# Performance work log

Hardware: AMD Instinct MI355X
Metric: run time of the kernel (lower is better)

## Reference

```python
import jax, jax.numpy as jnp
import numpy as np

EPS = 1e-05


def setup_inputs() -> dict:
    key = jax.random.key(0)
    k1, k2, k3 = jax.random.split(key, 3)
    B, M, W, H = 256, 8192, 32, 4
    memory = jax.random.normal(k1, (B, M, W), dtype=jnp.float32)
    keys = jax.random.normal(k2, (B, H, W), dtype=jnp.float32)
    strengths = jax.random.normal(k3, (B, H), dtype=jnp.float32)
    return {"memory": memory, "keys": keys, "strengths": strengths}


def reference(memory, keys, strengths):
    # memory: [B, M, W], keys: [B, H, W], strengths: [B, H]
    dot = jnp.einsum('bhw,bmw->bhm', keys, memory)          # [B, H, M]
    mem_norms = jnp.sqrt(jnp.sum(memory * memory, axis=-1) + EPS)  # [B, M]
    key_norms = jnp.sqrt(jnp.sum(keys * keys, axis=-1) + EPS)      # [B, H]
    norm = key_norms[:, :, None] * mem_norms[:, None, :]    # [B, H, M]
    activations = dot / (norm + EPS)
    sharp = activations * jax.nn.softplus(strengths)[:, :, None]
    # BatchSoftmax: legacy F.softmax on 2D [H, M] slices -> softmax over M
    return jax.nn.softmax(sharp, axis=-1)
```

## Files before the change

kernel.cpp:

```cpp
#include <hip/hip_runtime.h>
#include <math.h>

#define EPS 1e-5f

constexpr int Mc = 8192;
constexpr int Wc = 32;
constexpr int Hc = 4;
constexpr int NT = 1024;
constexpr int LD = Mc + 8;

__global__ __launch_bounds__(NT, 4) void weightfn_kernel(
    const float* __restrict__ memory,
    const float* __restrict__ keys,
    const float* __restrict__ strengths,
    float* __restrict__ out)
{
    __shared__ __align__(16) float s_sharp[Hc * LD];
    __shared__ __align__(16) float s_key[Hc * Wc];
    __shared__ float s_kn[Hc];
    __shared__ float s_beta[Hc];
    __shared__ float s_redm[NT / 64][Hc];
    __shared__ float s_redl[NT / 64][Hc];
    __shared__ float s_max[Hc];
    __shared__ float s_inv[Hc];

    const int b = blockIdx.x;
    const int t = threadIdx.x;

    if (t < Hc * Wc) s_key[t] = keys[(size_t)b * Hc * Wc + t];
    __syncthreads();
    if (t < Hc) {
        float s = 0.f;
        #pragma unroll
        for (int w = 0; w < Wc; ++w) { float k = s_key[t * Wc + w]; s += k * k; }
        s_kn[t] = sqrtf(s + EPS);
        float x = strengths[(size_t)b * Hc + t];
        s_beta[t] = fmaxf(x, 0.f) + log1pf(expf(-fabsf(x)));
    }
    __syncthreads();

    const int w4 = t & 7;
    const int mg = t >> 3;
    const float4* mp = reinterpret_cast<const float4*>(memory) + (size_t)b * (Mc * Wc / 4);
    const float4* kp = reinterpret_cast<const float4*>(s_key);
    const float4 k0 = kp[0 * 8 + w4];
    const float4 k1 = kp[1 * 8 + w4];
    const float4 k2 = kp[2 * 8 + w4];
    const float4 k3 = kp[3 * 8 + w4];
    const float myKn   = s_kn[w4 & 3];
    const float myBeta = s_beta[w4 & 3];

    #pragma unroll 4
    for (int k = 0; k < Mc / (NT / 8); ++k) {
        const int m = mg + k * (NT / 8);
        float4 v = mp[t + k * NT];
        float sq = v.x * v.x + v.y * v.y + v.z * v.z + v.w * v.w;
        float d0 = v.x * k0.x + v.y * k0.y + v.z * k0.z + v.w * k0.w;
        float d1 = v.x * k1.x + v.y * k1.y + v.z * k1.z + v.w * k1.w;
        float d2 = v.x * k2.x + v.y * k2.y + v.z * k2.z + v.w * k2.w;
        float d3 = v.x * k3.x + v.y * k3.y + v.z * k3.z + v.w * k3.w;
        #pragma unroll
        for (int off = 1; off <= 4; off <<= 1) {
            sq += __shfl_xor(sq, off);
            d0 += __shfl_xor(d0, off);
            d1 += __shfl_xor(d1, off);
            d2 += __shfl_xor(d2, off);
            d3 += __shfl_xor(d3, off);
        }
        if (w4 < Hc) {
            float d = (w4 == 0) ? d0 : (w4 == 1) ? d1 : (w4 == 2) ? d2 : d3;
            float mn = sqrtf(sq + EPS);
            s_sharp[w4 * LD + m] = d * myBeta / (myKn * mn + EPS);
        }
    }
    __syncthreads();

    const int wave = t >> 6;
    const int lane = t & 63;
    float mx[Hc];
    #pragma unroll
    for (int h = 0; h < Hc; ++h) mx[h] = -INFINITY;
    #pragma unroll
    for (int k = 0; k < Mc / NT; ++k) {
        const int m = t + k * NT;
        #pragma unroll
        for (int h = 0; h < Hc; ++h) mx[h] = fmaxf(mx[h], s_sharp[h * LD + m]);
    }
    #pragma unroll
    for (int off = 1; off < 64; off <<= 1) {
        #pragma unroll
        for (int h = 0; h < Hc; ++h) mx[h] = fmaxf(mx[h], __shfl_xor(mx[h], off));
    }
    if (lane == 0) {
        #pragma unroll
        for (int h = 0; h < Hc; ++h) s_redm[wave][h] = mx[h];
    }
    __syncthreads();
    if (t < Hc) {
        float m0 = s_redm[0][t];
        #pragma unroll
        for (int i = 1; i < NT / 64; ++i) m0 = fmaxf(m0, s_redm[i][t]);
        s_max[t] = m0;
    }
    __syncthreads();

    float gm[Hc];
    #pragma unroll
    for (int h = 0; h < Hc; ++h) gm[h] = s_max[h];
    float ls[Hc];
    #pragma unroll
    for (int h = 0; h < Hc; ++h) ls[h] = 0.f;
    #pragma unroll
    for (int k = 0; k < Mc / NT; ++k) {
        const int m = t + k * NT;
        #pragma unroll
        for (int h = 0; h < Hc; ++h) ls[h] += expf(s_sharp[h * LD + m] - gm[h]);
    }
    #pragma unroll
    for (int off = 1; off < 64; off <<= 1) {
        #pragma unroll
        for (int h = 0; h < Hc; ++h) ls[h] += __shfl_xor(ls[h], off);
    }
    if (lane == 0) {
        #pragma unroll
        for (int h = 0; h < Hc; ++h) s_redl[wave][h] = ls[h];
    }
    __syncthreads();
    if (t < Hc) {
        float s = 0.f;
        #pragma unroll
        for (int i = 0; i < NT / 64; ++i) s += s_redl[i][t];
        s_inv[t] = 1.f / s;
    }
    __syncthreads();

    float4* op = reinterpret_cast<float4*>(out) + (size_t)b * (Hc * Mc / 4);
    #pragma unroll
    for (int k = 0; k < (Hc * Mc / 4) / NT; ++k) {
        const int f = t + k * NT;
        const int h = f >> 11;
        const int r = f & 2047;
        float4 v = *reinterpret_cast<const float4*>(&s_sharp[h * LD + r * 4]);
        const float gmh = s_max[h];
        const float gih = s_inv[h];
        float4 o;
        o.x = expf(v.x - gmh) * gih;
        o.y = expf(v.y - gmh) * gih;
        o.z = expf(v.z - gmh) * gih;
        o.w = expf(v.w - gmh) * gih;
        op[f] = o;
    }
}

extern "C" void kernel_launch(void* const* d_in, const int* in_sizes, int n_in,
                              void* d_out, int out_size, void* d_ws, size_t ws_size,
                              hipStream_t stream) {
    const float* memory    = (const float*)d_in[0];
    const float* keys      = (const float*)d_in[1];
    const float* strengths = (const float*)d_in[2];
    float* out = (float*)d_out;

    const int B = in_sizes[0] / (Mc * Wc);
    dim3 grid(B), block(NT);
    hipLaunchKernelGGL(weightfn_kernel, grid, block, 0, stream,
                       memory, keys, strengths, out);
}
```

Baseline: 380.2 us.

## Drop softmax max pass by exploiting bounded cosine-similarity logits

Computes exp of the sharpened cosine similarity directly in the dot-product loop and accumulates the per-head sum there, removing the max-reduction pass, the separate sum pass, and the exp in the output pass. This relies on cosine similarity being bounded in [-1,1] so exp(beta*cos) stays in range when softplus(strength) is moderate. It could overflow for very large strengths. Fast-math intrinsics (__expf, rcp) replace expf and division, trading a little precision for fewer instructions.

```diff
diff --git a/kernel.cpp b/kernel.cpp
--- a/kernel.cpp
+++ b/kernel.cpp
@@ -19,9 +19,7 @@
     __shared__ __align__(16) float s_key[Hc * Wc];
     __shared__ float s_kn[Hc];
     __shared__ float s_beta[Hc];
-    __shared__ float s_redm[NT / 64][Hc];
     __shared__ float s_redl[NT / 64][Hc];
-    __shared__ float s_max[Hc];
     __shared__ float s_inv[Hc];
 
     const int b = blockIdx.x;
@@ -50,6 +48,8 @@
     const float myKn   = s_kn[w4 & 3];
     const float myBeta = s_beta[w4 & 3];
 
+    float esum = 0.f;
+
     #pragma unroll 4
     for (int k = 0; k < Mc / (NT / 8); ++k) {
         const int m = mg + k * (NT / 8);
@@ -70,67 +70,22 @@
         if (w4 < Hc) {
             float d = (w4 == 0) ? d0 : (w4 == 1) ? d1 : (w4 == 2) ? d2 : d3;
             float mn = sqrtf(sq + EPS);
-            s_sharp[w4 * LD + m] = d * myBeta / (myKn * mn + EPS);
+            float e = __expf(d * myBeta * __builtin_amdgcn_rcpf(myKn * mn + EPS));
+            s_sharp[w4 * LD + m] = e;
+            esum += e;
         }
     }
-    __syncthreads();
 
     const int wave = t >> 6;
-    const int lane = t & 63;
-    float mx[Hc];
     #pragma unroll
-    for (int h = 0; h < Hc; ++h) mx[h] = -INFINITY;
-    #pragma unroll
-    for (int k = 0; k < Mc / NT; ++k) {
-        const int m = t + k * NT;
-        #pragma unroll
-        for (int h = 0; h < Hc; ++h) mx[h] = fmaxf(mx[h], s_sharp[h * LD + m]);
-    }
-    #pragma unroll
-    for (int off = 1; off < 64; off <<= 1) {
-        #pragma unroll
-        for (int h = 0; h < Hc; ++h) mx[h] = fmaxf(mx[h], __shfl_xor(mx[h], off));
-    }
-    if (lane == 0) {
-        #pragma unroll
-        for (int h = 0; h < Hc; ++h) s_redm[wave][h] = mx[h];
-    }
-    __syncthreads();
-    if (t < Hc) {
-        float m0 = s_redm[0][t];
-        #pragma unroll
-        for (int i = 1; i < NT / 64; ++i) m0 = fmaxf(m0, s_redm[i][t]);
-        s_max[t] = m0;
-    }
-    __syncthreads();
-
-    float gm[Hc];
-    #pragma unroll
-    for (int h = 0; h < Hc; ++h) gm[h] = s_max[h];
-    float ls[Hc];
-    #pragma unroll
-    for (int h = 0; h < Hc; ++h) ls[h] = 0.f;
-    #pragma unroll
-    for (int k = 0; k < Mc / NT; ++k) {
-        const int m = t + k * NT;
-        #pragma unroll
-        for (int h = 0; h < Hc; ++h) ls[h] += expf(s_sharp[h * LD + m] - gm[h]);
-    }
-    #pragma unroll
-    for (int off = 1; off < 64; off <<= 1) {
-        #pragma unroll
-        for (int h = 0; h < Hc; ++h) ls[h] += __shfl_xor(ls[h], off);
-    }
-    if (lane == 0) {
-        #pragma unroll
-        for (int h = 0; h < Hc; ++h) s_redl[wave][h] = ls[h];
-    }
+    for (int off = 8; off <= 32; off <<= 1) esum += __shfl_xor(esum, off);
+    if ((t & 63) < Hc) s_redl[wave][w4] = esum;
     __syncthreads();
     if (t < Hc) {
         float s = 0.f;
         #pragma unroll
         for (int i = 0; i < NT / 64; ++i) s += s_redl[i][t];
-        s_inv[t] = 1.f / s;
+        s_inv[t] = __builtin_amdgcn_rcpf(s);
     }
     __syncthreads();
 
@@ -141,13 +96,12 @@
         const int h = f >> 11;
         const int r = f & 2047;
         float4 v = *reinterpret_cast<const float4*>(&s_sharp[h * LD + r * 4]);
-        const float gmh = s_max[h];
         const float gih = s_inv[h];
         float4 o;
-        o.x = expf(v.x - gmh) * gih;
-        o.y = expf(v.y - gmh) * gih;
-        o.z = expf(v.z - gmh) * gih;
-        o.w = expf(v.w - gmh) * gih;
+        o.x = v.x * gih;
+        o.y = v.y * gih;
+        o.z = v.z * gih;
+        o.w = v.w * gih;
         op[f] = o;
     }
 }
```

Result: no change. 376.7 us (-0.9%).
